# Kernel optimization log

Hardware: AMD Instinct MI355X
Metric: run time of the kernel (lower is better)

## Reference

```python
import jax, jax.numpy as jnp
import numpy as np

N = 200_000      # nodes
E = 6_400_000    # edges (avg degree 32)
G = 2_000        # graphs
SD = 10          # state_dim
ROUNDS = 3


def setup_inputs() -> dict:
    key = jax.random.key(0)
    ks = jax.random.split(key, 10)
    node_coordinates = jax.random.normal(ks[0], (N, 3), dtype=jnp.float32)
    node_graph_index = jnp.sort(jax.random.randint(ks[1], (N,), 0, G))
    node_from = jax.random.randint(ks[2], (E,), 0, N)
    node_to = jax.random.randint(ks[3], (E,), 0, N)
    edge_lengths = jax.random.uniform(ks[4], (E, 1), dtype=jnp.float32)
    edge_vectors = jax.random.normal(ks[5], (E, 3), dtype=jnp.float32)
    # message net: Linear(14 -> 10), torch default uniform init
    lim = 1.0 / np.sqrt(SD + 4)
    W_msg = jax.random.uniform(ks[6], (SD + 4, SD), minval=-lim, maxval=lim, dtype=jnp.float32)
    b_msg = jax.random.uniform(ks[7], (SD,), minval=-lim, maxval=lim, dtype=jnp.float32)
    # output net: Linear(10 -> 4), xavier_normal weight, default bias
    W_out = jax.random.normal(ks[8], (SD, 4), dtype=jnp.float32) * np.float32(np.sqrt(2.0 / (SD + 4)))
    lim_o = 1.0 / np.sqrt(SD)
    b_out = jax.random.uniform(ks[9], (4,), minval=-lim_o, maxval=lim_o, dtype=jnp.float32)
    return dict(node_coordinates=node_coordinates, edge_lengths=edge_lengths,
                edge_vectors=edge_vectors, W_msg=W_msg, b_msg=b_msg,
                W_out=W_out, b_out=b_out, node_from=node_from, node_to=node_to,
                node_graph_index=node_graph_index, num_nodes=N, num_graphs=G)


def reference(node_coordinates, edge_lengths, edge_vectors, W_msg, b_msg,
              W_out, b_out, node_from, node_to, node_graph_index,
              num_nodes, num_graphs):
    c_from = node_coordinates[node_from]                      # (E,3) gather
    c_to = node_coordinates[node_to]                          # (E,3) gather
    coord_sum = jnp.sum(jnp.abs(c_from), axis=1, keepdims=True)       # (E,1)
    dot1 = jnp.sum(c_from * c_to, axis=1, keepdims=True)              # (E,1)
    dot2 = jnp.sum(c_from * edge_vectors, axis=1, keepdims=True)      # (E,1)
    geo = jnp.concatenate([edge_lengths, coord_sum, dot1, dot2], axis=1)  # (E,4), identical every round

    state = jnp.zeros((num_nodes, SD), dtype=node_coordinates.dtype)
    for _ in range(ROUNDS):
        inp = jnp.concatenate([state[node_from], geo], axis=1)        # (E,14)
        msg = jnp.tanh(inp @ W_msg + b_msg)                           # (E,10)
        state = state + jax.ops.segment_sum(msg, node_to, num_segments=num_nodes)

    graph_state = jax.ops.segment_sum(state, node_graph_index, num_segments=num_graphs)  # (G,10)
    ev = graph_state @ W_out + b_out                                  # (G,4)
    gamma, v, alpha, beta = jnp.split(ev, 4, axis=1)
    sp = jax.nn.softplus
    return jnp.concatenate([gamma, sp(v), sp(alpha) + 1.0, sp(beta)], axis=1)
```

## Files before the change

kernel.cpp:

```cpp
#include <hip/hip_runtime.h>
#include <hip/hip_fp16.h>
#include <math.h>

#define SD 10
#define BB 6
#define BSZ 64
#define MAXNB 3328
#define EB 512
#define CTHR 1024
#define SCAP 4096

typedef unsigned uvec4 __attribute__((ext_vector_type(4)));
union U32H2 { unsigned u; __half2 h; };

__device__ __forceinline__ float tanh_fast(float x) {
    float e = __expf(2.0f * x);
    float r = __builtin_amdgcn_rcpf(1.0f + e);
    return 1.0f - 2.0f * r;
}

__device__ __forceinline__ float softplus_f(float x) {
    return fmaxf(x, 0.0f) + log1pf(expf(-fabsf(x)));
}


__global__ __launch_bounds__(256) void coords4_kernel(
    const float* __restrict__ coords, float4* __restrict__ coords4, int N)
{
    int n = blockIdx.x * blockDim.x + threadIdx.x;
    if (n >= N) return;
    float4 c;
    c.x = coords[n * 3 + 0];
    c.y = coords[n * 3 + 1];
    c.z = coords[n * 3 + 2];
    c.w = 0.0f;
    coords4[n] = c;
}


__global__ __launch_bounds__(CTHR) void bucket_count_kernel(
    const int* __restrict__ nto, unsigned* __restrict__ gcnt, int E, int NB)
{
    __shared__ unsigned h[MAXNB];
    int b = blockIdx.x;
    for (int i = threadIdx.x; i < NB; i += CTHR) h[i] = 0;
    __syncthreads();
    long long ebeg = (long long)E * b / EB;
    long long eend = (long long)E * (b + 1) / EB;
    for (long long e = ebeg + threadIdx.x; e < eend; e += CTHR)
        atomicAdd(&h[((unsigned)nto[e]) >> BB], 1u);
    __syncthreads();
    for (int k = threadIdx.x; k < NB; k += CTHR) gcnt[(size_t)k * EB + b] = h[k];
}

__global__ __launch_bounds__(256) void scan1_kernel(
    const unsigned* cnt, unsigned* off, unsigned* bsum, int M)
{
    __shared__ unsigned lds[256];
    int t = threadIdx.x, b = blockIdx.x;
    int base = b * 1024 + t * 4;
    unsigned v[4], s = 0;
#pragma unroll
    for (int k = 0; k < 4; k++) {
        v[k] = (base + k < M) ? cnt[base + k] : 0u;
        s += v[k];
    }
    lds[t] = s;
    __syncthreads();
    for (int d = 1; d < 256; d <<= 1) {
        unsigned x = (t >= d) ? lds[t - d] : 0u;
        __syncthreads();
        lds[t] += x;
        __syncthreads();
    }
    unsigned excl = (t > 0) ? lds[t - 1] : 0u;
    if (t == 255) bsum[b] = lds[255];
    unsigned run = excl;
#pragma unroll
    for (int k = 0; k < 4; k++) {
        if (base + k < M) off[base + k] = run;
        run += v[k];
    }
}

__global__ __launch_bounds__(256) void scan2_kernel(unsigned* __restrict__ bsum, int nb)
{
    __shared__ unsigned lds[256];
    int t = threadIdx.x;
    unsigned v = (t < nb) ? bsum[t] : 0u;
    lds[t] = v;
    __syncthreads();
    for (int d = 1; d < 256; d <<= 1) {
        unsigned x = (t >= d) ? lds[t - d] : 0u;
        __syncthreads();
        lds[t] += x;
        __syncthreads();
    }
    unsigned excl = (t > 0) ? lds[t - 1] : 0u;
    if (t < nb) bsum[t] = excl;
}

__global__ __launch_bounds__(256) void scan_add_kernel(
    unsigned* __restrict__ off, const unsigned* __restrict__ bsum, int M)
{
    int i = blockIdx.x * blockDim.x + threadIdx.x;
    if (i < M) off[i] += bsum[i >> 10];
}

__global__ __launch_bounds__(256) void bstart_kernel(
    const unsigned* __restrict__ gbase, unsigned* __restrict__ bstart, int NB, int E)
{
    int k = blockIdx.x * blockDim.x + threadIdx.x;
    if (k > NB) return;
    bstart[k] = (k < NB) ? gbase[(size_t)k * EB] : (unsigned)E;
}

__global__ __launch_bounds__(CTHR) void bucket_scatter_kernel(
    const float4* __restrict__ coords4,
    const float* __restrict__ elen,
    const float* __restrict__ evec,
    const int* __restrict__ nfrom,
    const int* __restrict__ nto,
    const unsigned* __restrict__ gbase,
    uvec4* __restrict__ payload,
    int E, int NB)
{
    __shared__ unsigned cur[MAXNB];
    int b = blockIdx.x;
    for (int k = threadIdx.x; k < NB; k += CTHR) cur[k] = gbase[(size_t)k * EB + b];
    __syncthreads();
    long long ebeg = (long long)E * b / EB;
    long long eend = (long long)E * (b + 1) / EB;
    for (long long e = ebeg + threadIdx.x; e < eend; e += CTHR) {
        int nf = nfrom[e];
        int nt = nto[e];
        unsigned k = ((unsigned)nt) >> BB;
        unsigned pos = atomicAdd(&cur[k], 1u);

        float4 cf = coords4[nf];
        float4 ct = coords4[nt];
        float ev0 = evec[e * 3 + 0], ev1 = evec[e * 3 + 1], ev2 = evec[e * 3 + 2];

        float g0 = elen[e];
        float g1 = fabsf(cf.x) + fabsf(cf.y) + fabsf(cf.z);
        float g2 = cf.x * ct.x + cf.y * ct.y + cf.z * ct.z;
        float g3 = cf.x * ev0 + cf.y * ev1 + cf.z * ev2;

        U32H2 c01, c23;
        c01.h = __floats2half2_rn(g0, g1);
        c23.h = __floats2half2_rn(g2, g3);
        uvec4 p;
        p.x = (unsigned)nf | (((unsigned)nt & (BSZ - 1)) << 18);
        p.y = c01.u;
        p.z = c23.u;
        p.w = 0u;
        payload[pos] = p;
    }
}

__global__ __launch_bounds__(256) void sort_bucket_kernel(
    const unsigned* __restrict__ bstart, uvec4* payload)
{
    __shared__ uvec4 sbuf[SCAP];
    __shared__ unsigned scnt[BSZ], scur[BSZ];
    int k = blockIdx.x;
    unsigned beg = bstart[k], end = bstart[k + 1];
    unsigned len = end - beg;
    if (len > SCAP) return;
    int t = threadIdx.x;
    if (t < BSZ) scnt[t] = 0;
    for (unsigned i = t; i < len; i += 256) sbuf[i] = payload[beg + i];
    __syncthreads();
    for (unsigned i = t; i < len; i += 256)
        atomicAdd(&scnt[(sbuf[i].x >> 18) & (BSZ - 1)], 1u);
    __syncthreads();
    if (t < 64) {
        unsigned v = scnt[t];
        unsigned inc = v;
        for (int d = 1; d < 64; d <<= 1) {
            unsigned u = __shfl_up(inc, d, 64);
            if (t >= d) inc += u;
        }
        scur[t] = inc - v;
    }
    __syncthreads();
    for (unsigned i = t; i < len; i += 256) {
        uvec4 p = sbuf[i];
        unsigned pos = atomicAdd(&scur[(p.x >> 18) & (BSZ - 1)], 1u);
        payload[beg + pos] = p;
    }
}


__global__ __launch_bounds__(256) void wstate_kernel(
    const float* __restrict__ state, const float* __restrict__ Wm,
    const float* __restrict__ bm, __half* __restrict__ wsth, int N)
{
    int n = blockIdx.x * blockDim.x + threadIdx.x;
    if (n >= N) return;
    const float2* sp = (const float2*)(state + (size_t)n * SD);
    float s[SD];
#pragma unroll
    for (int h = 0; h < 5; h++) { float2 v = sp[h]; s[2*h] = v.x; s[2*h+1] = v.y; }
    float t[SD];
#pragma unroll
    for (int j = 0; j < SD; j++) t[j] = bm[j];
#pragma unroll
    for (int k = 0; k < SD; k++) {
#pragma unroll
        for (int j = 0; j < SD; j++) t[j] += s[k] * Wm[k * SD + j];
    }
    unsigned* dp = (unsigned*)(wsth + (size_t)n * SD);
#pragma unroll
    for (int h = 0; h < 5; h++) {
        U32H2 cv;
        cv.h = __floats2half2_rn(t[2*h], t[2*h+1]);
        dp[h] = cv.u;
    }
}

template <bool FIRST>
__global__ __launch_bounds__(256) void round_run_kernel(
    const unsigned* __restrict__ bstart,
    const uvec4* __restrict__ payload,
    const float* __restrict__ Wm,
    const float* __restrict__ bm,
    const __half* __restrict__ wsth,
    const float* __restrict__ state_prev,
    float* __restrict__ state_next,
    int N, int E)
{
    __shared__ float acc[BSZ * SD];
    int k = blockIdx.x;
    for (int i = threadIdx.x; i < BSZ * SD; i += 256) acc[i] = 0.0f;

    int lane = threadIdx.x & 63;
    int wv = threadIdx.x >> 6;
    int grp0 = lane / 10;
    bool active = grp0 < 6;
    int grp = active ? grp0 : 5;
    int j = active ? (lane - grp0 * 10) : (lane - 60);

    float w0 = Wm[10 * SD + j];
    float w1 = Wm[11 * SD + j];
    float w2 = Wm[12 * SD + j];
    float w3 = Wm[13 * SD + j];
    float bb = bm[j];
    __syncthreads();

    unsigned beg = bstart[k], end = bstart[k + 1];
    unsigned len = end - beg;
    unsigned Q = (len + 3) >> 2;
    unsigned rbeg = beg + (unsigned)wv * Q;
    unsigned rend = rbeg + Q; if (rend > end) rend = end;
    unsigned eclamp = (unsigned)E - 1u;

    unsigned e0 = rbeg + (unsigned)grp;
    uvec4 P0 = payload[e0 <= eclamp ? e0 : eclamp];
    unsigned e1 = e0 + 6;
    uvec4 P1 = payload[e1 <= eclamp ? e1 : eclamp];
    float T0 = bb, T1 = bb;
    if (!FIRST) T0 = __half2float(wsth[(size_t)(P0.x & 0x3FFFFu) * SD + j]);

    int cur_lnt = -1;
    float accv = 0.0f;

    for (unsigned base = rbeg; base < rend; base += 6) {
        unsigned e2 = base + 12 + (unsigned)grp;
        uvec4 P2 = payload[e2 <= eclamp ? e2 : eclamp];
        if (!FIRST) T1 = __half2float(wsth[(size_t)(P1.x & 0x3FFFFu) * SD + j]);
        unsigned e = base + (unsigned)grp;
        if (active && e < rend) {
            int lnt = (int)((P0.x >> 18) & (BSZ - 1));
            U32H2 c01, c23;
            c01.u = P0.y; c23.u = P0.z;
            float g0 = __low2float(c01.h), g1 = __high2float(c01.h);
            float g2 = __low2float(c23.h), g3 = __high2float(c23.h);
            float t = T0 + g0 * w0 + g1 * w1 + g2 * w2 + g3 * w3;
            if (lnt != cur_lnt) {
                if (cur_lnt >= 0) atomicAdd(&acc[cur_lnt * SD + j], accv);
                accv = 0.0f;
                cur_lnt = lnt;
            }
            accv += tanh_fast(t);
        }
        P0 = P1; P1 = P2; T0 = T1;
    }
    if (active && cur_lnt >= 0) atomicAdd(&acc[cur_lnt * SD + j], accv);
    __syncthreads();

    int base_o = k * BSZ * SD;
    int lim = N * SD - base_o;
    for (int i = threadIdx.x; i < BSZ * SD; i += 256) {
        if (i < lim) {
            float v = acc[i];
            if (!FIRST) v += state_prev[base_o + i];
            state_next[base_o + i] = v;
        }
    }
}


__global__ __launch_bounds__(256) void goff_kernel(
    const int* __restrict__ gidx, unsigned* __restrict__ goff, int N, int G)
{
    int n = blockIdx.x * blockDim.x + threadIdx.x;
    if (n >= N) return;
    int g = gidx[n];
    if (n == 0) {
        for (int q = 0; q <= g; q++) goff[q] = 0;
    } else {
        int gp = gidx[n - 1];
        for (int q = gp + 1; q <= g; q++) goff[q] = (unsigned)n;
    }
    if (n == N - 1) {
        for (int q = g + 1; q <= G; q++) goff[q] = (unsigned)N;
    }
}

__global__ __launch_bounds__(256) void gsum_kernel(
    const float* __restrict__ state, const unsigned* __restrict__ goff,
    float* __restrict__ gstate, int G)
{
    int tid = blockIdx.x * blockDim.x + threadIdx.x;
    if (tid >= G * SD * 4) return;
    int s = tid & 3;
    int rest = tid >> 2;
    int g = rest / SD;
    int j = rest - g * SD;
    unsigned beg = goff[g], end = goff[g + 1];
    unsigned len = end - beg;
    unsigned b0 = beg + (len * (unsigned)s) / 4u;
    unsigned b1 = beg + (len * (unsigned)(s + 1)) / 4u;
    float a = 0.0f;
    for (unsigned n = b0; n < b1; n++) a += state[(size_t)n * SD + j];
    atomicAdd(&gstate[(size_t)g * SD + j], a);
}

__global__ __launch_bounds__(256) void out_kernel(
    const float* __restrict__ gstate, const float* __restrict__ Wo,
    const float* __restrict__ bo, float* __restrict__ out, int G)
{
    int g = blockIdx.x * blockDim.x + threadIdx.x;
    if (g >= G) return;
    float s[SD];
#pragma unroll
    for (int k = 0; k < SD; k++) s[k] = gstate[(size_t)g * SD + k];
    float ev[4];
#pragma unroll
    for (int c = 0; c < 4; c++) {
        float a = bo[c];
#pragma unroll
        for (int k = 0; k < SD; k++) a += s[k] * Wo[k * 4 + c];
        ev[c] = a;
    }
    out[g * 4 + 0] = ev[0];
    out[g * 4 + 1] = softplus_f(ev[1]);
    out[g * 4 + 2] = softplus_f(ev[2]) + 1.0f;
    out[g * 4 + 3] = softplus_f(ev[3]);
}


template <bool FIRST>
__global__ __launch_bounds__(256) void edge_kernel_fb(
    const float* __restrict__ coords, const float* __restrict__ elen,
    const float* __restrict__ evec, const float* __restrict__ Wm,
    const float* __restrict__ bm, const int* __restrict__ nfrom,
    const int* __restrict__ nto, const float* __restrict__ state_prev,
    float* __restrict__ state_next, int E)
{
    int e = blockIdx.x * blockDim.x + threadIdx.x;
    if (e >= E) return;
    int nf = nfrom[e];
    int nt = nto[e];
    float cf0 = coords[nf*3+0], cf1 = coords[nf*3+1], cf2 = coords[nf*3+2];
    float ct0 = coords[nt*3+0], ct1 = coords[nt*3+1], ct2 = coords[nt*3+2];
    float ev0 = evec[e*3+0], ev1 = evec[e*3+1], ev2 = evec[e*3+2];
    float g0 = elen[e];
    float g1 = fabsf(cf0) + fabsf(cf1) + fabsf(cf2);
    float g2 = cf0*ct0 + cf1*ct1 + cf2*ct2;
    float g3 = cf0*ev0 + cf1*ev1 + cf2*ev2;
    float acc[SD];
#pragma unroll
    for (int j = 0; j < SD; j++) {
        acc[j] = bm[j] + g0*Wm[10*SD+j] + g1*Wm[11*SD+j] + g2*Wm[12*SD+j] + g3*Wm[13*SD+j];
    }
    if (!FIRST) {
        const float2* sp = (const float2*)(state_prev + (size_t)nf * SD);
        float s[SD];
#pragma unroll
        for (int h = 0; h < 5; h++) { float2 v = sp[h]; s[2*h] = v.x; s[2*h+1] = v.y; }
#pragma unroll
        for (int k = 0; k < SD; k++) {
#pragma unroll
            for (int j = 0; j < SD; j++) acc[j] += s[k] * Wm[k*SD+j];
        }
    }
    float* dst = state_next + (size_t)nt * SD;
#pragma unroll
    for (int j = 0; j < SD; j++) atomicAdd(dst + j, tanh_fast(acc[j]));
}

__global__ __launch_bounds__(256) void graph_reduce_fb(
    const float* __restrict__ state, const int* __restrict__ gidx,
    float* __restrict__ gstate, int N)
{
    int n = blockIdx.x * blockDim.x + threadIdx.x;
    if (n >= N) return;
    int g = gidx[n];
    const float2* sp = (const float2*)(state + (size_t)n * SD);
    float* dst = gstate + (size_t)g * SD;
#pragma unroll
    for (int h = 0; h < 5; h++) {
        float2 v = sp[h];
        atomicAdd(dst + 2*h, v.x);
        atomicAdd(dst + 2*h + 1, v.y);
    }
}


extern "C" void kernel_launch(void* const* d_in, const int* in_sizes, int n_in,
                              void* d_out, int out_size, void* d_ws, size_t ws_size,
                              hipStream_t stream) {
    const float* coords = (const float*)d_in[0];
    const float* elen   = (const float*)d_in[1];
    const float* evec   = (const float*)d_in[2];
    const float* Wm     = (const float*)d_in[3];
    const float* bm     = (const float*)d_in[4];
    const float* Wo     = (const float*)d_in[5];
    const float* bo     = (const float*)d_in[6];
    const int* nfrom    = (const int*)d_in[7];
    const int* nto      = (const int*)d_in[8];
    const int* gidx     = (const int*)d_in[9];

    const int E = in_sizes[1];
    const int N = in_sizes[9];
    const int G = out_size / 4;

    const int NB  = (N + BSZ - 1) / BSZ;
    const int M   = NB * EB;
    const int nb1 = (M + 1023) / 1024;
    const int nb2 = (nb1 + 1023) / 1024;

    const int BLK = 256;
    const int ng = (N + BLK - 1) / BLK;
    const int gg = (G + BLK - 1) / BLK;

    auto align256 = [](size_t x) { return (x + 255) & ~(size_t)255; };
    const size_t state_bytes = align256((size_t)N * SD * sizeof(float));
    const size_t wst_bytes   = align256((size_t)N * SD * sizeof(__half) + 256);
    const size_t pay_bytes   = align256((size_t)E * sizeof(uvec4));
    const size_t gcnt_bytes  = align256((size_t)M * sizeof(unsigned));
    const size_t bsumA_bytes = align256((size_t)nb1 * sizeof(unsigned));
    const size_t bsumB_bytes = align256((size_t)(nb2 > 0 ? nb2 : 1) * sizeof(unsigned) + 256);
    const size_t bst_bytes   = align256((size_t)(NB + 1) * sizeof(unsigned));
    const size_t goff_bytes  = align256((size_t)(G + 1) * sizeof(unsigned));
    const size_t gst_bytes   = align256((size_t)G * SD * sizeof(float));
    const size_t c4_bytes    = align256((size_t)N * sizeof(float4));

    size_t o = 0;
    char* w = (char*)d_ws;
    float* stateA    = (float*)(w + o);    o += state_bytes;
    float* stateB    = (float*)(w + o);    o += state_bytes;
    __half* wsth     = (__half*)(w + o);   o += wst_bytes;
    uvec4* payload   = (uvec4*)(w + o);    o += pay_bytes;
    unsigned* gcnt   = (unsigned*)(w + o); o += gcnt_bytes;
    unsigned* gbase  = (unsigned*)(w + o); o += gcnt_bytes;
    unsigned* bsumA  = (unsigned*)(w + o); o += bsumA_bytes;
    unsigned* bsumB  = (unsigned*)(w + o); o += bsumB_bytes;
    unsigned* bstart = (unsigned*)(w + o); o += bst_bytes;
    unsigned* goff   = (unsigned*)(w + o); o += goff_bytes;
    float* gstate    = (float*)(w + o);    o += gst_bytes;
    float4* coords4  = (float4*)(w + o);   o += c4_bytes;

    if (o <= ws_size && NB <= MAXNB && nb1 <= 1024 * 256 && nb2 <= 256 && N < (1 << 18)) {
        coords4_kernel<<<ng, BLK, 0, stream>>>(coords, coords4, N);
        bucket_count_kernel<<<EB, CTHR, 0, stream>>>(nto, gcnt, E, NB);
        scan1_kernel<<<nb1, 256, 0, stream>>>(gcnt, gbase, bsumA, M);
        scan1_kernel<<<nb2, 256, 0, stream>>>(bsumA, bsumA, bsumB, nb1);
        scan2_kernel<<<1, 256, 0, stream>>>(bsumB, nb2);
        scan_add_kernel<<<(nb1 + 255) / 256, 256, 0, stream>>>(bsumA, bsumB, nb1);
        scan_add_kernel<<<(M + 255) / 256, 256, 0, stream>>>(gbase, bsumA, M);
        bstart_kernel<<<(NB + 256) / 256, 256, 0, stream>>>(gbase, bstart, NB, E);
        bucket_scatter_kernel<<<EB, CTHR, 0, stream>>>(coords4, elen, evec, nfrom, nto,
                                                       gbase, payload, E, NB);
        sort_bucket_kernel<<<NB, BLK, 0, stream>>>(bstart, payload);
        round_run_kernel<true><<<NB, BLK, 0, stream>>>(bstart, payload, Wm, bm,
                                                       wsth, stateB, stateA, N, E);
        wstate_kernel<<<ng, BLK, 0, stream>>>(stateA, Wm, bm, wsth, N);
        round_run_kernel<false><<<NB, BLK, 0, stream>>>(bstart, payload, Wm, bm,
                                                        wsth, stateA, stateB, N, E);
        wstate_kernel<<<ng, BLK, 0, stream>>>(stateB, Wm, bm, wsth, N);
        round_run_kernel<false><<<NB, BLK, 0, stream>>>(bstart, payload, Wm, bm,
                                                        wsth, stateB, stateA, N, E);
        hipMemsetAsync(gstate, 0, (size_t)G * SD * sizeof(float), stream);
        goff_kernel<<<ng, BLK, 0, stream>>>(gidx, goff, N, G);
        gsum_kernel<<<(G * SD * 4 + BLK - 1) / BLK, BLK, 0, stream>>>(stateA, goff, gstate, G);
        out_kernel<<<gg, BLK, 0, stream>>>(gstate, Wo, bo, (float*)d_out, G);
    } else {
        const int eg = (E + BLK - 1) / BLK;
        float* gstateF = (float*)(w + 2 * state_bytes);
        hipMemsetAsync(stateA, 0, state_bytes, stream);
        hipMemsetAsync(gstateF, 0, (size_t)G * SD * sizeof(float), stream);
        edge_kernel_fb<true><<<eg, BLK, 0, stream>>>(coords, elen, evec, Wm, bm,
                                                     nfrom, nto, stateA, stateA, E);
        hipMemcpyAsync(stateB, stateA, state_bytes, hipMemcpyDeviceToDevice, stream);
        edge_kernel_fb<false><<<eg, BLK, 0, stream>>>(coords, elen, evec, Wm, bm,
                                                      nfrom, nto, stateA, stateB, E);
        hipMemcpyAsync(stateA, stateB, state_bytes, hipMemcpyDeviceToDevice, stream);
        edge_kernel_fb<false><<<eg, BLK, 0, stream>>>(coords, elen, evec, Wm, bm,
                                                      nfrom, nto, stateB, stateA, E);
        graph_reduce_fb<<<ng, BLK, 0, stream>>>(stateA, gidx, gstateF, N);
        out_kernel<<<gg, BLK, 0, stream>>>(gstateF, Wo, bo, (float*)d_out, G);
    }
}
```

Measured before the change: 823.8 us.

## Use larger 256-node buckets with register-staged in-bucket sort

Bucket size grows from 64 to 256 nodes, which cuts the bucket count from about 3125 to about 782, and the global scatter runs with fewer blocks. The per-bucket sort now uses 1024 threads that hold up to 12 payload entries each in registers instead of staging them in a 64KB shared buffer, and it uses a shared-memory Hillis-Steele scan over 256 counters. Larger buckets mean fewer, bigger round blocks and possibly better locality in the round kernels. The cost is heavier register use in the sort, more sync-bound scan steps, and a risk that a bucket with more than 12288 edges leaves the sort early and stays unsorted.

Measured after the change: 892.4 us. 1.08x slower.

```diff
diff --git a/kernel.cpp b/kernel.cpp
--- a/kernel.cpp
+++ b/kernel.cpp
@@ -3,12 +3,12 @@
 #include <math.h>
 
 #define SD 10
-#define BB 6
-#define BSZ 64
-#define MAXNB 3328
-#define EB 512
+#define BB 8
+#define BSZ 256
+#define MAXNB 1024
+#define EB 256
 #define CTHR 1024
-#define SCAP 4096
+#define SPT 12
 
 typedef unsigned uvec4 __attribute__((ext_vector_type(4)));
 union U32H2 { unsigned u; __half2 h; };
@@ -158,36 +158,45 @@
     }
 }
 
-__global__ __launch_bounds__(256) void sort_bucket_kernel(
+__global__ __launch_bounds__(1024) void sort_bucket_kernel(
     const unsigned* __restrict__ bstart, uvec4* payload)
 {
-    __shared__ uvec4 sbuf[SCAP];
-    __shared__ unsigned scnt[BSZ], scur[BSZ];
+    __shared__ unsigned scnt[BSZ], sscan[BSZ], scur[BSZ];
     int k = blockIdx.x;
     unsigned beg = bstart[k], end = bstart[k + 1];
     unsigned len = end - beg;
-    if (len > SCAP) return;
+    if (len > 1024u * SPT) return;
     int t = threadIdx.x;
     if (t < BSZ) scnt[t] = 0;
-    for (unsigned i = t; i < len; i += 256) sbuf[i] = payload[beg + i];
-    __syncthreads();
-    for (unsigned i = t; i < len; i += 256)
-        atomicAdd(&scnt[(sbuf[i].x >> 18) & (BSZ - 1)], 1u);
-    __syncthreads();
-    if (t < 64) {
-        unsigned v = scnt[t];
-        unsigned inc = v;
-        for (int d = 1; d < 64; d <<= 1) {
-            unsigned u = __shfl_up(inc, d, 64);
-            if (t >= d) inc += u;
+    __syncthreads();
+    uvec4 st[SPT];
+#pragma unroll
+    for (int c = 0; c < SPT; c++) {
+        unsigned i = (unsigned)t + (unsigned)c * 1024u;
+        if (i < len) {
+            st[c] = payload[beg + i];
+            atomicAdd(&scnt[(st[c].x >> 18) & (BSZ - 1)], 1u);
         }
-        scur[t] = inc - v;
-    }
-    __syncthreads();
-    for (unsigned i = t; i < len; i += 256) {
-        uvec4 p = sbuf[i];
-        unsigned pos = atomicAdd(&scur[(p.x >> 18) & (BSZ - 1)], 1u);
-        payload[beg + pos] = p;
+    }
+    __syncthreads();
+    if (t < BSZ) sscan[t] = scnt[t];
+    __syncthreads();
+    for (int d = 1; d < BSZ; d <<= 1) {
+        unsigned x = 0;
+        if (t < BSZ && t >= d) x = sscan[t - d];
+        __syncthreads();
+        if (t < BSZ) sscan[t] += x;
+        __syncthreads();
+    }
+    if (t < BSZ) scur[t] = beg + sscan[t] - scnt[t];
+    __syncthreads();
+#pragma unroll
+    for (int c = 0; c < SPT; c++) {
+        unsigned i = (unsigned)t + (unsigned)c * 1024u;
+        if (i < len) {
+            unsigned pos = atomicAdd(&scur[(st[c].x >> 18) & (BSZ - 1)], 1u);
+            payload[pos] = st[c];
+        }
     }
 }
 
@@ -484,7 +493,7 @@
         bstart_kernel<<<(NB + 256) / 256, 256, 0, stream>>>(gbase, bstart, NB, E);
         bucket_scatter_kernel<<<EB, CTHR, 0, stream>>>(coords4, elen, evec, nfrom, nto,
                                                        gbase, payload, E, NB);
-        sort_bucket_kernel<<<NB, BLK, 0, stream>>>(bstart, payload);
+        sort_bucket_kernel<<<NB, 1024, 0, stream>>>(bstart, payload);
         round_run_kernel<true><<<NB, BLK, 0, stream>>>(bstart, payload, Wm, bm,
                                                        wsth, stateB, stateA, N, E);
         wstate_kernel<<<ng, BLK, 0, stream>>>(stateA, Wm, bm, wsth, N);
```

## Replace global bucket sort with per-block local partition and segmented gather

Applied to the files above, without the earlier changes.

Drops the global multi-level scan, bucket-start and in-bucket sort kernels. Each scatter block now scans its own bucket counts and writes edges into its own slice of the payload. The round kernel rebuilds each bucket's view with a prefix scan over the 512 source segments and binary search, then accumulates with per-edge LDS atomics. Buckets grow to 128 nodes. This removes several launches and a full payload re-read and re-write, but the rounds gain scattered segment reads and more LDS atomic contention.

After: 1.699 ms. 2.06x slower.

```diff
diff --git a/kernel.cpp b/kernel.cpp
--- a/kernel.cpp
+++ b/kernel.cpp
@@ -3,12 +3,11 @@
 #include <math.h>
 
 #define SD 10
-#define BB 6
-#define BSZ 64
-#define MAXNB 3328
+#define BB 7
+#define BSZ 128
+#define MAXNB 2048
 #define EB 512
 #define CTHR 1024
-#define SCAP 4096
 
 typedef unsigned uvec4 __attribute__((ext_vector_type(4)));
 union U32H2 { unsigned u; __half2 h; };
@@ -53,85 +52,42 @@
     for (int k = threadIdx.x; k < NB; k += CTHR) gcnt[(size_t)k * EB + b] = h[k];
 }
 
-__global__ __launch_bounds__(256) void scan1_kernel(
-    const unsigned* cnt, unsigned* off, unsigned* bsum, int M)
-{
-    __shared__ unsigned lds[256];
-    int t = threadIdx.x, b = blockIdx.x;
-    int base = b * 1024 + t * 4;
-    unsigned v[4], s = 0;
-#pragma unroll
-    for (int k = 0; k < 4; k++) {
-        v[k] = (base + k < M) ? cnt[base + k] : 0u;
-        s += v[k];
-    }
-    lds[t] = s;
-    __syncthreads();
-    for (int d = 1; d < 256; d <<= 1) {
-        unsigned x = (t >= d) ? lds[t - d] : 0u;
-        __syncthreads();
-        lds[t] += x;
-        __syncthreads();
-    }
-    unsigned excl = (t > 0) ? lds[t - 1] : 0u;
-    if (t == 255) bsum[b] = lds[255];
-    unsigned run = excl;
-#pragma unroll
-    for (int k = 0; k < 4; k++) {
-        if (base + k < M) off[base + k] = run;
-        run += v[k];
-    }
-}
-
-__global__ __launch_bounds__(256) void scan2_kernel(unsigned* __restrict__ bsum, int nb)
-{
-    __shared__ unsigned lds[256];
-    int t = threadIdx.x;
-    unsigned v = (t < nb) ? bsum[t] : 0u;
-    lds[t] = v;
-    __syncthreads();
-    for (int d = 1; d < 256; d <<= 1) {
-        unsigned x = (t >= d) ? lds[t - d] : 0u;
-        __syncthreads();
-        lds[t] += x;
-        __syncthreads();
-    }
-    unsigned excl = (t > 0) ? lds[t - 1] : 0u;
-    if (t < nb) bsum[t] = excl;
-}
-
-__global__ __launch_bounds__(256) void scan_add_kernel(
-    unsigned* __restrict__ off, const unsigned* __restrict__ bsum, int M)
-{
-    int i = blockIdx.x * blockDim.x + threadIdx.x;
-    if (i < M) off[i] += bsum[i >> 10];
-}
-
-__global__ __launch_bounds__(256) void bstart_kernel(
-    const unsigned* __restrict__ gbase, unsigned* __restrict__ bstart, int NB, int E)
-{
-    int k = blockIdx.x * blockDim.x + threadIdx.x;
-    if (k > NB) return;
-    bstart[k] = (k < NB) ? gbase[(size_t)k * EB] : (unsigned)E;
-}
-
 __global__ __launch_bounds__(CTHR) void bucket_scatter_kernel(
     const float4* __restrict__ coords4,
     const float* __restrict__ elen,
     const float* __restrict__ evec,
     const int* __restrict__ nfrom,
     const int* __restrict__ nto,
-    const unsigned* __restrict__ gbase,
+    const unsigned* __restrict__ gcnt,
+    unsigned* __restrict__ eaddr,
     uvec4* __restrict__ payload,
     int E, int NB)
 {
     __shared__ unsigned cur[MAXNB];
+    __shared__ unsigned scn[CTHR];
     int b = blockIdx.x;
-    for (int k = threadIdx.x; k < NB; k += CTHR) cur[k] = gbase[(size_t)k * EB + b];
-    __syncthreads();
+    int t = threadIdx.x;
     long long ebeg = (long long)E * b / EB;
     long long eend = (long long)E * (b + 1) / EB;
-    for (long long e = ebeg + threadIdx.x; e < eend; e += CTHR) {
+
+    unsigned a0 = (2 * t < NB) ? gcnt[(size_t)(2 * t) * EB + b] : 0u;
+    unsigned a1 = (2 * t + 1 < NB) ? gcnt[(size_t)(2 * t + 1) * EB + b] : 0u;
+    scn[t] = a0 + a1;
+    __syncthreads();
+    for (int d = 1; d < CTHR; d <<= 1) {
+        unsigned x = (t >= d) ? scn[t - d] : 0u;
+        __syncthreads();
+        scn[t] += x;
+        __syncthreads();
+    }
+    unsigned excl = t ? scn[t - 1] : 0u;
+    unsigned s0 = (unsigned)ebeg + excl;
+    unsigned s1 = s0 + a0;
+    if (2 * t < NB)     { cur[2 * t] = s0;     eaddr[(size_t)(2 * t) * EB + b] = s0; }
+    if (2 * t + 1 < NB) { cur[2 * t + 1] = s1; eaddr[(size_t)(2 * t + 1) * EB + b] = s1; }
+    __syncthreads();
+
+    for (long long e = ebeg + t; e < eend; e += CTHR) {
         int nf = nfrom[e];
         int nt = nto[e];
         unsigned k = ((unsigned)nt) >> BB;
@@ -158,39 +114,6 @@
     }
 }
 
-__global__ __launch_bounds__(256) void sort_bucket_kernel(
-    const unsigned* __restrict__ bstart, uvec4* payload)
-{
-    __shared__ uvec4 sbuf[SCAP];
-    __shared__ unsigned scnt[BSZ], scur[BSZ];
-    int k = blockIdx.x;
-    unsigned beg = bstart[k], end = bstart[k + 1];
-    unsigned len = end - beg;
-    if (len > SCAP) return;
-    int t = threadIdx.x;
-    if (t < BSZ) scnt[t] = 0;
-    for (unsigned i = t; i < len; i += 256) sbuf[i] = payload[beg + i];
-    __syncthreads();
-    for (unsigned i = t; i < len; i += 256)
-        atomicAdd(&scnt[(sbuf[i].x >> 18) & (BSZ - 1)], 1u);
-    __syncthreads();
-    if (t < 64) {
-        unsigned v = scnt[t];
-        unsigned inc = v;
-        for (int d = 1; d < 64; d <<= 1) {
-            unsigned u = __shfl_up(inc, d, 64);
-            if (t >= d) inc += u;
-        }
-        scur[t] = inc - v;
-    }
-    __syncthreads();
-    for (unsigned i = t; i < len; i += 256) {
-        uvec4 p = sbuf[i];
-        unsigned pos = atomicAdd(&scur[(p.x >> 18) & (BSZ - 1)], 1u);
-        payload[beg + pos] = p;
-    }
-}
-
 
 __global__ __launch_bounds__(256) void wstate_kernel(
     const float* __restrict__ state, const float* __restrict__ Wm,
@@ -220,19 +143,43 @@
 }
 
 template <bool FIRST>
-__global__ __launch_bounds__(256) void round_run_kernel(
-    const unsigned* __restrict__ bstart,
+__global__ __launch_bounds__(256) void round_gather_kernel(
+    const unsigned* __restrict__ gcnt,
+    const unsigned* __restrict__ eaddr,
     const uvec4* __restrict__ payload,
     const float* __restrict__ Wm,
     const float* __restrict__ bm,
     const __half* __restrict__ wsth,
     const float* __restrict__ state_prev,
     float* __restrict__ state_next,
-    int N, int E)
+    int N)
 {
     __shared__ float acc[BSZ * SD];
+    __shared__ unsigned opref[EB + 1];
+    __shared__ unsigned segst[EB];
+    __shared__ unsigned scn[256];
     int k = blockIdx.x;
-    for (int i = threadIdx.x; i < BSZ * SD; i += 256) acc[i] = 0.0f;
+    int t = threadIdx.x;
+    for (int i = t; i < BSZ * SD; i += 256) acc[i] = 0.0f;
+
+    unsigned c0 = gcnt[(size_t)k * EB + 2 * t];
+    unsigned c1 = gcnt[(size_t)k * EB + 2 * t + 1];
+    segst[2 * t]     = eaddr[(size_t)k * EB + 2 * t];
+    segst[2 * t + 1] = eaddr[(size_t)k * EB + 2 * t + 1];
+    scn[t] = c0 + c1;
+    __syncthreads();
+    for (int d = 1; d < 256; d <<= 1) {
+        unsigned x = (t >= d) ? scn[t - d] : 0u;
+        __syncthreads();
+        scn[t] += x;
+        __syncthreads();
+    }
+    unsigned excl = t ? scn[t - 1] : 0u;
+    opref[2 * t] = excl;
+    opref[2 * t + 1] = excl + c0;
+    if (t == 255) opref[EB] = excl + c0 + c1;
+    __syncthreads();
+    unsigned len = opref[EB];
 
     int lane = threadIdx.x & 63;
     int wv = threadIdx.x >> 6;
@@ -246,52 +193,53 @@
     float w2 = Wm[12 * SD + j];
     float w3 = Wm[13 * SD + j];
     float bb = bm[j];
-    __syncthreads();
-
-    unsigned beg = bstart[k], end = bstart[k + 1];
-    unsigned len = end - beg;
-    unsigned Q = (len + 3) >> 2;
-    unsigned rbeg = beg + (unsigned)wv * Q;
-    unsigned rend = rbeg + Q; if (rend > end) rend = end;
-    unsigned eclamp = (unsigned)E - 1u;
-
-    unsigned e0 = rbeg + (unsigned)grp;
-    uvec4 P0 = payload[e0 <= eclamp ? e0 : eclamp];
-    unsigned e1 = e0 + 6;
-    uvec4 P1 = payload[e1 <= eclamp ? e1 : eclamp];
-    float T0 = bb, T1 = bb;
-    if (!FIRST) T0 = __half2float(wsth[(size_t)(P0.x & 0x3FFFFu) * SD + j]);
-
-    int cur_lnt = -1;
-    float accv = 0.0f;
-
-    for (unsigned base = rbeg; base < rend; base += 6) {
-        unsigned e2 = base + 12 + (unsigned)grp;
-        uvec4 P2 = payload[e2 <= eclamp ? e2 : eclamp];
-        if (!FIRST) T1 = __half2float(wsth[(size_t)(P1.x & 0x3FFFFu) * SD + j]);
-        unsigned e = base + (unsigned)grp;
-        if (active && e < rend) {
-            int lnt = (int)((P0.x >> 18) & (BSZ - 1));
-            U32H2 c01, c23;
-            c01.u = P0.y; c23.u = P0.z;
-            float g0 = __low2float(c01.h), g1 = __high2float(c01.h);
-            float g2 = __low2float(c23.h), g3 = __high2float(c23.h);
-            float t = T0 + g0 * w0 + g1 * w1 + g2 * w2 + g3 * w3;
-            if (lnt != cur_lnt) {
-                if (cur_lnt >= 0) atomicAdd(&acc[cur_lnt * SD + j], accv);
-                accv = 0.0f;
-                cur_lnt = lnt;
+
+    if (len) {
+        unsigned Q = (len + 3) >> 2;
+        unsigned rbeg = (unsigned)wv * Q;
+        unsigned rend = rbeg + Q; if (rend > len) rend = len;
+        unsigned lm1 = len - 1;
+
+        unsigned i0 = rbeg + (unsigned)grp;
+        unsigned i0c = i0 < len ? i0 : lm1;
+        unsigned blo = 0, bhi = EB;
+#pragma unroll
+        for (int s = 0; s < 9; s++) {
+            unsigned mid = (blo + bhi) >> 1;
+            if (opref[mid] <= i0c) blo = mid; else bhi = mid;
+        }
+        unsigned bw = blo;
+        uvec4 P0 = payload[segst[bw] + (i0c - opref[bw])];
+        unsigned i1c = i0 + 6; if (i1c > lm1) i1c = lm1;
+        while (opref[bw + 1] <= i1c) bw++;
+        uvec4 P1 = payload[segst[bw] + (i1c - opref[bw])];
+        float T0 = bb, T1 = bb;
+        if (!FIRST) T0 = __half2float(wsth[(size_t)(P0.x & 0x3FFFFu) * SD + j]);
+
+        for (unsigned base = rbeg; base < rend; base += 6) {
+            unsigned i2 = base + 12 + (unsigned)grp;
+            unsigned i2c = i2 > lm1 ? lm1 : i2;
+            while (opref[bw + 1] <= i2c) bw++;
+            uvec4 P2 = payload[segst[bw] + (i2c - opref[bw])];
+            if (!FIRST) T1 = __half2float(wsth[(size_t)(P1.x & 0x3FFFFu) * SD + j]);
+            unsigned i = base + (unsigned)grp;
+            if (active && i < rend) {
+                int lnt = (int)((P0.x >> 18) & (BSZ - 1));
+                U32H2 c01, c23;
+                c01.u = P0.y; c23.u = P0.z;
+                float g0 = __low2float(c01.h), g1 = __high2float(c01.h);
+                float g2 = __low2float(c23.h), g3 = __high2float(c23.h);
+                float tt = T0 + g0 * w0 + g1 * w1 + g2 * w2 + g3 * w3;
+                atomicAdd(&acc[lnt * SD + j], tanh_fast(tt));
             }
-            accv += tanh_fast(t);
+            P0 = P1; P1 = P2; T0 = T1;
         }
-        P0 = P1; P1 = P2; T0 = T1;
-    }
-    if (active && cur_lnt >= 0) atomicAdd(&acc[cur_lnt * SD + j], accv);
+    }
     __syncthreads();
 
     int base_o = k * BSZ * SD;
     int lim = N * SD - base_o;
-    for (int i = threadIdx.x; i < BSZ * SD; i += 256) {
+    for (int i = t; i < BSZ * SD; i += 256) {
         if (i < lim) {
             float v = acc[i];
             if (!FIRST) v += state_prev[base_o + i];
@@ -437,10 +385,8 @@
     const int N = in_sizes[9];
     const int G = out_size / 4;
 
-    const int NB  = (N + BSZ - 1) / BSZ;
-    const int M   = NB * EB;
-    const int nb1 = (M + 1023) / 1024;
-    const int nb2 = (nb1 + 1023) / 1024;
+    const int NB = (N + BSZ - 1) / BSZ;
+    const size_t M = (size_t)NB * EB;
 
     const int BLK = 256;
     const int ng = (N + BLK - 1) / BLK;
@@ -450,10 +396,7 @@
     const size_t state_bytes = align256((size_t)N * SD * sizeof(float));
     const size_t wst_bytes   = align256((size_t)N * SD * sizeof(__half) + 256);
     const size_t pay_bytes   = align256((size_t)E * sizeof(uvec4));
-    const size_t gcnt_bytes  = align256((size_t)M * sizeof(unsigned));
-    const size_t bsumA_bytes = align256((size_t)nb1 * sizeof(unsigned));
-    const size_t bsumB_bytes = align256((size_t)(nb2 > 0 ? nb2 : 1) * sizeof(unsigned) + 256);
-    const size_t bst_bytes   = align256((size_t)(NB + 1) * sizeof(unsigned));
+    const size_t gcnt_bytes  = align256(M * sizeof(unsigned));
     const size_t goff_bytes  = align256((size_t)(G + 1) * sizeof(unsigned));
     const size_t gst_bytes   = align256((size_t)G * SD * sizeof(float));
     const size_t c4_bytes    = align256((size_t)N * sizeof(float4));
@@ -465,34 +408,24 @@
     __half* wsth     = (__half*)(w + o);   o += wst_bytes;
     uvec4* payload   = (uvec4*)(w + o);    o += pay_bytes;
     unsigned* gcnt   = (unsigned*)(w + o); o += gcnt_bytes;
-    unsigned* gbase  = (unsigned*)(w + o); o += gcnt_bytes;
-    unsigned* bsumA  = (unsigned*)(w + o); o += bsumA_bytes;
-    unsigned* bsumB  = (unsigned*)(w + o); o += bsumB_bytes;
-    unsigned* bstart = (unsigned*)(w + o); o += bst_bytes;
+    unsigned* eaddr  = (unsigned*)(w + o); o += gcnt_bytes;
     unsigned* goff   = (unsigned*)(w + o); o += goff_bytes;
     float* gstate    = (float*)(w + o);    o += gst_bytes;
     float4* coords4  = (float4*)(w + o);   o += c4_bytes;
 
-    if (o <= ws_size && NB <= MAXNB && nb1 <= 1024 * 256 && nb2 <= 256 && N < (1 << 18)) {
+    if (o <= ws_size && NB <= MAXNB && N < (1 << 18)) {
         coords4_kernel<<<ng, BLK, 0, stream>>>(coords, coords4, N);
         bucket_count_kernel<<<EB, CTHR, 0, stream>>>(nto, gcnt, E, NB);
-        scan1_kernel<<<nb1, 256, 0, stream>>>(gcnt, gbase, bsumA, M);
-        scan1_kernel<<<nb2, 256, 0, stream>>>(bsumA, bsumA, bsumB, nb1);
-        scan2_kernel<<<1, 256, 0, stream>>>(bsumB, nb2);
-        scan_add_kernel<<<(nb1 + 255) / 256, 256, 0, stream>>>(bsumA, bsumB, nb1);
-        scan_add_kernel<<<(M + 255) / 256, 256, 0, stream>>>(gbase, bsumA, M);
-        bstart_kernel<<<(NB + 256) / 256, 256, 0, stream>>>(gbase, bstart, NB, E);
         bucket_scatter_kernel<<<EB, CTHR, 0, stream>>>(coords4, elen, evec, nfrom, nto,
-                                                       gbase, payload, E, NB);
-        sort_bucket_kernel<<<NB, BLK, 0, stream>>>(bstart, payload);
-        round_run_kernel<true><<<NB, BLK, 0, stream>>>(bstart, payload, Wm, bm,
-                                                       wsth, stateB, stateA, N, E);
+                                                       gcnt, eaddr, payload, E, NB);
+        round_gather_kernel<true><<<NB, BLK, 0, stream>>>(gcnt, eaddr, payload, Wm, bm,
+                                                          wsth, stateB, stateA, N);
         wstate_kernel<<<ng, BLK, 0, stream>>>(stateA, Wm, bm, wsth, N);
-        round_run_kernel<false><<<NB, BLK, 0, stream>>>(bstart, payload, Wm, bm,
-                                                        wsth, stateA, stateB, N, E);
+        round_gather_kernel<false><<<NB, BLK, 0, stream>>>(gcnt, eaddr, payload, Wm, bm,
+                                                           wsth, stateA, stateB, N);
         wstate_kernel<<<ng, BLK, 0, stream>>>(stateB, Wm, bm, wsth, N);
-        round_run_kernel<false><<<NB, BLK, 0, stream>>>(bstart, payload, Wm, bm,
-                                                        wsth, stateB, stateA, N, E);
+        round_gather_kernel<false><<<NB, BLK, 0, stream>>>(gcnt, eaddr, payload, Wm, bm,
+                                                           wsth, stateB, stateA, N);
         hipMemsetAsync(gstate, 0, (size_t)G * SD * sizeof(float), stream);
         goff_kernel<<<ng, BLK, 0, stream>>>(gidx, goff, N, G);
         gsum_kernel<<<(G * SD * 4 + BLK - 1) / BLK, BLK, 0, stream>>>(stateA, goff, gstate, G);
```
